# Kernel optimization log

Hardware: AMD Instinct MI355X
Metric: run time of the kernel (lower is better)

Reference implementation:

```python
import jax, jax.numpy as jnp
import numpy as np

N_HEAD = 8
N_INPUTS = 2
N_EMBD = 256
B, T1, T2 = 4, 8192, 8192


def setup_inputs() -> dict:
    key = jax.random.key(0)
    ks = jax.random.split(key, 8)
    s = 1.0 / np.sqrt(N_EMBD)
    return {
        "x": jax.random.normal(ks[0], (B, T1, N_EMBD), dtype=jnp.float32),
        "y": jax.random.normal(ks[1], (N_INPUTS, B, T2, N_EMBD), dtype=jnp.float32),
        "Wq": jax.random.normal(ks[2], (N_EMBD, N_EMBD), dtype=jnp.float32) * s,
        "bq": jnp.zeros((N_EMBD,), dtype=jnp.float32),
        "Wk": jax.random.normal(ks[3], (N_INPUTS, N_EMBD, N_EMBD), dtype=jnp.float32) * s,
        "bk": jnp.zeros((N_INPUTS, N_EMBD), dtype=jnp.float32),
        "Wv": jax.random.normal(ks[4], (N_INPUTS, N_EMBD, N_EMBD), dtype=jnp.float32) * s,
        "bv": jnp.zeros((N_INPUTS, N_EMBD), dtype=jnp.float32),
        "Wp": jax.random.normal(ks[5], (N_EMBD, N_EMBD), dtype=jnp.float32) * s,
        "bp": jnp.zeros((N_EMBD,), dtype=jnp.float32),
    }


def _split_heads(t):
    # [B, T, C] -> [B, H, T, d]
    Bt, Tt, C = t.shape
    return t.reshape(Bt, Tt, N_HEAD, C // N_HEAD).transpose(0, 2, 1, 3)


def reference(x, y, Wq, bq, Wk, bk, Wv, bv, Wp, bp):
    Bx, T, C = x.shape
    q = jax.nn.softmax(_split_heads(x @ Wq + bq), axis=-1)  # [B,H,T1,d]
    out = q  # faithful to original: out initialized to q
    for i in range(N_INPUTS):
        k = jax.nn.softmax(_split_heads(y[i] @ Wk[i] + bk[i]), axis=-1)  # [B,H,T2,d]
        v = _split_heads(y[i] @ Wv[i] + bv[i])                            # [B,H,T2,d]
        k_cumsum = k.sum(axis=-2, keepdims=True)                          # [B,H,1,d]
        D_inv = 1.0 / (q * k_cumsum).sum(axis=-1, keepdims=True)          # [B,H,T1,1]
        kv = jnp.einsum('bhtd,bhte->bhde', k, v)                          # [B,H,d,d]
        out = out + jnp.einsum('bhnd,bhde->bhne', q, kv) * D_inv
    # b h n d -> b n (h d)
    out = out.transpose(0, 2, 1, 3).reshape(Bx, T, C)
    return out @ Wp + bp
```

## Files before the change

### kernel.cpp

```cpp
#include <hip/hip_runtime.h>
#include <math.h>

#define NHEAD 8
#define CEMB  256
#define NIN   2
#define BB    4
#define TT    8192

typedef __attribute__((ext_vector_type(8))) short short8;
typedef __attribute__((ext_vector_type(4))) float f32x4;
typedef __attribute__((ext_vector_type(16))) float f32x16;

__device__ __forceinline__ unsigned short f2bf(float f) {
    union { float f; unsigned u; } v; v.f = f;
    unsigned u = v.u;
    return (unsigned short)((u + 0x7fffu + ((u >> 16) & 1u)) >> 16);
}
__device__ __forceinline__ float bf2f(unsigned short s) {
    union { unsigned u; float f; } v; v.u = ((unsigned)s) << 16;
    return v.f;
}

__global__ __launch_bounds__(256) void prep_w(const float* __restrict__ Wq,
    const float* __restrict__ Wk, const float* __restrict__ Wv,
    const float* __restrict__ Wp, unsigned short* __restrict__ wsb)
{
    int gid = blockIdx.x * 256 + threadIdx.x;
    int m = gid >> 16;
    int idx = gid & 65535;
    int n = idx >> 8, k = idx & 255;
    const float* src; unsigned short* dst;
    switch (m) {
        case 0: src = Wq;          dst = wsb;          break;
        case 1: src = Wk;          dst = wsb + 65536;  break;
        case 2: src = Wk + 65536;  dst = wsb + 131072; break;
        case 3: src = Wv;          dst = wsb + 196608; break;
        case 4: src = Wv + 65536;  dst = wsb + 262144; break;
        default: src = Wp;         dst = wsb + 327680; break;
    }
    dst[n * 256 + k] = f2bf(src[k * 256 + n]);
}

template<int ITERS>
__global__ __launch_bounds__(512, 2) void passA(const float* __restrict__ y,
    const float* __restrict__ bk, const float* __restrict__ bv,
    const unsigned short* __restrict__ Wkt, const unsigned short* __restrict__ Wvt,
    float* __restrict__ part)
{
    __shared__ unsigned short ytile[64][256];
    __shared__ unsigned short tr[8][32][68];

    const int i = blockIdx.z, b = blockIdx.y, x0 = blockIdx.x;
    const int tid = threadIdx.x;
    const int wid = tid >> 6, lane = tid & 63;
    const int lg = lane >> 4, li = lane & 15;
    const int l31 = lane & 31, hk = lane >> 5;
    const int h = wid, lm = li & 7;

    const float bk0 = bk[i * CEMB + h * 32 + li];
    const float bk1 = bk[i * CEMB + h * 32 + 16 + li];
    const float bv0 = bv[i * CEMB + h * 32 + li];
    const float bv1 = bv[i * CEMB + h * 32 + 16 + li];

    const unsigned short* wk0 = Wkt + ((size_t)(i * 256 + h * 32 + li)) * 256 + lg * 8;
    const unsigned short* wk1 = wk0 + 16 * 256;
    const unsigned short* wv0 = Wvt + ((size_t)(i * 256 + h * 32 + li)) * 256 + lg * 8;
    const unsigned short* wv1 = wv0 + 16 * 256;

    f32x16 kvacc = {};
    float ksa0 = 0.f, ksa1 = 0.f;

    #pragma unroll
    for (int iter = 0; iter < ITERS; ++iter) {
        __syncthreads();
        const int row0 = (x0 * ITERS + iter) * 64;
        const float* yb = y + ((size_t)(i * BB + b) * TT + row0) * CEMB;
        #pragma unroll
        for (int j = 0; j < 8; ++j) {
            int idx = tid + j * 512;
            int r = idx >> 6, c4 = (idx & 63) << 2;
            int sw = ((((c4 >> 3) ^ (r & 7)) << 3) | (c4 & 7));
            float4 v4 = *(const float4*)&yb[(size_t)r * CEMB + c4];
            ushort4 p; p.x = f2bf(v4.x); p.y = f2bf(v4.y); p.z = f2bf(v4.z); p.w = f2bf(v4.w);
            *(ushort4*)&ytile[r][sw] = p;
        }
        __syncthreads();

        f32x4 acc[4][2];
        #pragma unroll
        for (int rt = 0; rt < 4; ++rt) { acc[rt][0] = (f32x4){}; acc[rt][1] = (f32x4){}; }
        #pragma unroll 2
        for (int ks = 0; ks < 8; ++ks) {
            const int sw8 = (((4 * ks + lg) ^ lm) << 3);
            short8 a0 = *(const short8*)&ytile[li][sw8];
            short8 a1 = *(const short8*)&ytile[16 + li][sw8];
            short8 a2 = *(const short8*)&ytile[32 + li][sw8];
            short8 a3 = *(const short8*)&ytile[48 + li][sw8];
            short8 f0 = *(const short8*)(wk0 + ks * 32);
            short8 f1 = *(const short8*)(wk1 + ks * 32);
            acc[0][0] = __builtin_amdgcn_mfma_f32_16x16x32_bf16(a0, f0, acc[0][0], 0, 0, 0);
            acc[0][1] = __builtin_amdgcn_mfma_f32_16x16x32_bf16(a0, f1, acc[0][1], 0, 0, 0);
            acc[1][0] = __builtin_amdgcn_mfma_f32_16x16x32_bf16(a1, f0, acc[1][0], 0, 0, 0);
            acc[1][1] = __builtin_amdgcn_mfma_f32_16x16x32_bf16(a1, f1, acc[1][1], 0, 0, 0);
            acc[2][0] = __builtin_amdgcn_mfma_f32_16x16x32_bf16(a2, f0, acc[2][0], 0, 0, 0);
            acc[2][1] = __builtin_amdgcn_mfma_f32_16x16x32_bf16(a2, f1, acc[2][1], 0, 0, 0);
            acc[3][0] = __builtin_amdgcn_mfma_f32_16x16x32_bf16(a3, f0, acc[3][0], 0, 0, 0);
            acc[3][1] = __builtin_amdgcn_mfma_f32_16x16x32_bf16(a3, f1, acc[3][1], 0, 0, 0);
        }
        #pragma unroll
        for (int rt = 0; rt < 4; ++rt) {
            float kq0[4], kq1[4];
            #pragma unroll
            for (int reg = 0; reg < 4; ++reg) {
                float e0 = __expf(acc[rt][0][reg] + bk0);
                float e1 = __expf(acc[rt][1][reg] + bk1);
                float s = e0 + e1;
                s += __shfl_xor(s, 1, 16);
                s += __shfl_xor(s, 2, 16);
                s += __shfl_xor(s, 4, 16);
                s += __shfl_xor(s, 8, 16);
                float isv = 1.f / s;
                kq0[reg] = e0 * isv; kq1[reg] = e1 * isv;
                ksa0 += kq0[reg]; ksa1 += kq1[reg];
            }
            ushort4 p;
            p.x = f2bf(kq0[0]); p.y = f2bf(kq0[1]); p.z = f2bf(kq0[2]); p.w = f2bf(kq0[3]);
            *(ushort4*)&tr[wid][li][16 * rt + 4 * lg] = p;
            p.x = f2bf(kq1[0]); p.y = f2bf(kq1[1]); p.z = f2bf(kq1[2]); p.w = f2bf(kq1[3]);
            *(ushort4*)&tr[wid][16 + li][16 * rt + 4 * lg] = p;
        }
        #pragma unroll
        for (int rt = 0; rt < 4; ++rt) { acc[rt][0] = (f32x4){}; acc[rt][1] = (f32x4){}; }
        #pragma unroll 2
        for (int ks = 0; ks < 8; ++ks) {
            const int sw8 = (((4 * ks + lg) ^ lm) << 3);
            short8 a0 = *(const short8*)&ytile[li][sw8];
            short8 a1 = *(const short8*)&ytile[16 + li][sw8];
            short8 a2 = *(const short8*)&ytile[32 + li][sw8];
            short8 a3 = *(const short8*)&ytile[48 + li][sw8];
            short8 f0 = *(const short8*)(wv0 + ks * 32);
            short8 f1 = *(const short8*)(wv1 + ks * 32);
            acc[0][0] = __builtin_amdgcn_mfma_f32_16x16x32_bf16(a0, f0, acc[0][0], 0, 0, 0);
            acc[0][1] = __builtin_amdgcn_mfma_f32_16x16x32_bf16(a0, f1, acc[0][1], 0, 0, 0);
            acc[1][0] = __builtin_amdgcn_mfma_f32_16x16x32_bf16(a1, f0, acc[1][0], 0, 0, 0);
            acc[1][1] = __builtin_amdgcn_mfma_f32_16x16x32_bf16(a1, f1, acc[1][1], 0, 0, 0);
            acc[2][0] = __builtin_amdgcn_mfma_f32_16x16x32_bf16(a2, f0, acc[2][0], 0, 0, 0);
            acc[2][1] = __builtin_amdgcn_mfma_f32_16x16x32_bf16(a2, f1, acc[2][1], 0, 0, 0);
            acc[3][0] = __builtin_amdgcn_mfma_f32_16x16x32_bf16(a3, f0, acc[3][0], 0, 0, 0);
            acc[3][1] = __builtin_amdgcn_mfma_f32_16x16x32_bf16(a3, f1, acc[3][1], 0, 0, 0);
        }
        asm volatile("s_waitcnt lgkmcnt(0)" ::: "memory");
        short8 ka[4];
        #pragma unroll
        for (int ts = 0; ts < 4; ++ts)
            ka[ts] = *(const short8*)&tr[wid][l31][ts * 16 + hk * 8];
        asm volatile("s_waitcnt lgkmcnt(0)" ::: "memory");
        #pragma unroll
        for (int rt = 0; rt < 4; ++rt) {
            ushort4 p;
            p.x = f2bf(acc[rt][0][0] + bv0); p.y = f2bf(acc[rt][0][1] + bv0);
            p.z = f2bf(acc[rt][0][2] + bv0); p.w = f2bf(acc[rt][0][3] + bv0);
            *(ushort4*)&tr[wid][li][16 * rt + 4 * lg] = p;
            p.x = f2bf(acc[rt][1][0] + bv1); p.y = f2bf(acc[rt][1][1] + bv1);
            p.z = f2bf(acc[rt][1][2] + bv1); p.w = f2bf(acc[rt][1][3] + bv1);
            *(ushort4*)&tr[wid][16 + li][16 * rt + 4 * lg] = p;
        }
        asm volatile("s_waitcnt lgkmcnt(0)" ::: "memory");
        #pragma unroll
        for (int ts = 0; ts < 4; ++ts) {
            short8 vb = *(const short8*)&tr[wid][l31][ts * 16 + hk * 8];
            kvacc = __builtin_amdgcn_mfma_f32_32x32x16_bf16(ka[ts], vb, kvacc, 0, 0, 0);
        }
        asm volatile("s_waitcnt lgkmcnt(0)" ::: "memory");
    }

    const int slots = TT / (ITERS * 64);
    const size_t slot = (size_t)(i * BB + b) * slots + x0;
    float* pb = part + slot * (NHEAD * 1056) + (size_t)h * 1056;
    #pragma unroll
    for (int reg = 0; reg < 16; ++reg) {
        int d = (reg & 3) + 8 * (reg >> 2) + 4 * hk;
        pb[d * 32 + l31] = kvacc[reg];
    }
    float s0 = ksa0, s1 = ksa1;
    s0 += __shfl_xor(s0, 16, 64); s0 += __shfl_xor(s0, 32, 64);
    s1 += __shfl_xor(s1, 16, 64); s1 += __shfl_xor(s1, 32, 64);
    if (lg == 0) { pb[1024 + li] = s0; pb[1024 + 16 + li] = s1; }
}

__global__ __launch_bounds__(256) void reduceKV1(const float* __restrict__ part,
    float* __restrict__ part2, int slots)
{
    const int sc = blockIdx.x, g = blockIdx.y;
    const int ib = g >> 3, h = g & 7;
    const int tid = threadIdx.x;
    const float* p = part + ((size_t)(ib * slots + sc * 8) * NHEAD + h) * 1056;
    float* o = part2 + ((size_t)(sc * 64 + g)) * 1056;
    const size_t sstride = (size_t)NHEAD * 1056;
    for (int e = tid; e < 1056; e += 256) {
        float s = 0.f;
        #pragma unroll
        for (int xx = 0; xx < 8; ++xx) s += p[(size_t)xx * sstride + e];
        o[e] = s;
    }
}

__global__ __launch_bounds__(256) void reduceKV2(const float* __restrict__ part2,
    unsigned short* __restrict__ kvt, float* __restrict__ ksum, int nsc)
{
    const int g = blockIdx.x;
    const int tid = threadIdx.x;
    const size_t gstride = (size_t)64 * 1056;
    const float* p = part2 + (size_t)g * 1056;
    for (int e = tid; e < 1056; e += 256) {
        float s = 0.f;
        for (int sc = 0; sc < nsc; ++sc) s += p[(size_t)sc * gstride + e];
        if (e < 1024) kvt[(size_t)g * 1024 + (e & 31) * 32 + (e >> 5)] = f2bf(s);
        else          ksum[(size_t)g * 32 + (e - 1024)] = s;
    }
}

__global__ __launch_bounds__(512, 4) void passB(const float* __restrict__ x,
    const float* __restrict__ bq, const float* __restrict__ bp,
    const unsigned short* __restrict__ Wqt, const unsigned short* __restrict__ Wpt,
    const unsigned short* __restrict__ kvt, const float* __restrict__ ksum,
    float* __restrict__ out)
{
    __shared__ unsigned short xa[64][256];
    __shared__ unsigned short ql[64][256];
    __shared__ float dl[2][64][8];

    const int b = blockIdx.y, x0 = blockIdx.x;
    const int row0 = x0 * 64;
    const int tid = threadIdx.x;
    const int wid = tid >> 6, lane = tid & 63, lg = lane >> 4, li = lane & 15;
    const int h = wid, lm = li & 7;

    const float* xb = x + ((size_t)b * TT + row0) * CEMB;
    #pragma unroll
    for (int j = 0; j < 8; ++j) {
        int idx = tid + j * 512;
        int r = idx >> 6, c4 = (idx & 63) << 2;
        int sw = ((((c4 >> 3) ^ (r & 7)) << 3) | (c4 & 7));
        float4 v4 = *(const float4*)&xb[(size_t)r * CEMB + c4];
        ushort4 p; p.x = f2bf(v4.x); p.y = f2bf(v4.y); p.z = f2bf(v4.z); p.w = f2bf(v4.w);
        *(ushort4*)&xa[r][sw] = p;
    }
    __syncthreads();

    {
        f32x4 qa[4][2];
        #pragma unroll
        for (int rt = 0; rt < 4; ++rt) { qa[rt][0] = (f32x4){}; qa[rt][1] = (f32x4){}; }

        const unsigned short* wq0 = Wqt + ((size_t)(h * 32 + li)) * 256 + lg * 8;
        const unsigned short* wq1 = wq0 + 16 * 256;
        #pragma unroll 2
        for (int ks = 0; ks < 8; ++ks) {
            const int sw8 = (((4 * ks + lg) ^ lm) << 3);
            short8 a0 = *(const short8*)&xa[li][sw8];
            short8 a1 = *(const short8*)&xa[16 + li][sw8];
            short8 a2 = *(const short8*)&xa[32 + li][sw8];
            short8 a3 = *(const short8*)&xa[48 + li][sw8];
            short8 f0 = *(const short8*)(wq0 + ks * 32);
            short8 f1 = *(const short8*)(wq1 + ks * 32);
            qa[0][0] = __builtin_amdgcn_mfma_f32_16x16x32_bf16(a0, f0, qa[0][0], 0, 0, 0);
            qa[0][1] = __builtin_amdgcn_mfma_f32_16x16x32_bf16(a0, f1, qa[0][1], 0, 0, 0);
            qa[1][0] = __builtin_amdgcn_mfma_f32_16x16x32_bf16(a1, f0, qa[1][0], 0, 0, 0);
            qa[1][1] = __builtin_amdgcn_mfma_f32_16x16x32_bf16(a1, f1, qa[1][1], 0, 0, 0);
            qa[2][0] = __builtin_amdgcn_mfma_f32_16x16x32_bf16(a2, f0, qa[2][0], 0, 0, 0);
            qa[2][1] = __builtin_amdgcn_mfma_f32_16x16x32_bf16(a2, f1, qa[2][1], 0, 0, 0);
            qa[3][0] = __builtin_amdgcn_mfma_f32_16x16x32_bf16(a3, f0, qa[3][0], 0, 0, 0);
            qa[3][1] = __builtin_amdgcn_mfma_f32_16x16x32_bf16(a3, f1, qa[3][1], 0, 0, 0);
        }
        const float bq0 = bq[h * 32 + li];
        const float bq1 = bq[h * 32 + 16 + li];
        #pragma unroll
        for (int rt = 0; rt < 4; ++rt) {
            #pragma unroll
            for (int reg = 0; reg < 4; ++reg) {
                float e0 = __expf(qa[rt][0][reg] + bq0);
                float e1 = __expf(qa[rt][1][reg] + bq1);
                float s = e0 + e1;
                s += __shfl_xor(s, 1, 16);
                s += __shfl_xor(s, 2, 16);
                s += __shfl_xor(s, 4, 16);
                s += __shfl_xor(s, 8, 16);
                float isv = 1.f / s;
                int r = 16 * rt + 4 * lg + reg;
                int r7 = r & 7;
                int sw0 = (((4 * h + (li >> 3)) ^ r7) << 3) | lm;
                int sw1 = (((4 * h + 2 + (li >> 3)) ^ r7) << 3) | lm;
                ql[r][sw0] = f2bf(e0 * isv);
                ql[r][sw1] = f2bf(e1 * isv);
            }
        }
    }
    __syncthreads();

    {
        int r = tid >> 3, hh = tid & 7;
        const float* ks0 = ksum + ((size_t)(0 * BB + b) * 8 + hh) * 32;
        const float* ks1 = ksum + ((size_t)(1 * BB + b) * 8 + hh) * 32;
        float s0 = 0.f, s1 = 0.f;
        #pragma unroll
        for (int d8 = 0; d8 < 4; ++d8) {
            int cu = (((4 * hh + d8) ^ (r & 7)) << 3);
            #pragma unroll
            for (int dd = 0; dd < 8; ++dd) {
                float qv = bf2f(ql[r][cu + dd]);
                s0 += qv * ks0[d8 * 8 + dd];
                s1 += qv * ks1[d8 * 8 + dd];
            }
        }
        dl[0][r][hh] = 1.f / s0;
        dl[1][r][hh] = 1.f / s1;
    }
    __syncthreads();

    #pragma unroll
    for (int rt = 0; rt < 4; ++rt) {
        float of0[4], of1[4];
        #pragma unroll
        for (int reg = 0; reg < 4; ++reg) {
            int rk = (4 * lg + reg) & 7;
            int r = 16 * rt + 4 * lg + reg;
            int col0 = (((4 * h + (li >> 3)) ^ rk) << 3) | lm;
            int col1 = (((4 * h + 2 + (li >> 3)) ^ rk) << 3) | lm;
            of0[reg] = bf2f(ql[r][col0]);
            of1[reg] = bf2f(ql[r][col1]);
        }
        short8 af = *(const short8*)&ql[16 * rt + li][(((4 * h + lg) ^ lm) << 3)];
        #pragma unroll
        for (int ii = 0; ii < NIN; ++ii) {
            const unsigned short* kvb = kvt + ((size_t)((ii * BB + b) * 8 + h)) * 1024;
            short8 b0 = *(const short8*)(kvb + (size_t)li * 32 + lg * 8);
            short8 b1 = *(const short8*)(kvb + (size_t)(16 + li) * 32 + lg * 8);
            f32x4 z = {};
            f32x4 t0 = __builtin_amdgcn_mfma_f32_16x16x32_bf16(af, b0, z, 0, 0, 0);
            f32x4 t1 = __builtin_amdgcn_mfma_f32_16x16x32_bf16(af, b1, z, 0, 0, 0);
            #pragma unroll
            for (int reg = 0; reg < 4; ++reg) {
                float dv = dl[ii][16 * rt + 4 * lg + reg][h];
                of0[reg] += t0[reg] * dv;
                of1[reg] += t1[reg] * dv;
            }
        }
        #pragma unroll
        for (int reg = 0; reg < 4; ++reg) {
            int rk = (4 * lg + reg) & 7;
            int r = 16 * rt + 4 * lg + reg;
            int col0 = (((4 * h + (li >> 3)) ^ rk) << 3) | lm;
            int col1 = (((4 * h + 2 + (li >> 3)) ^ rk) << 3) | lm;
            xa[r][col0] = f2bf(of0[reg]);
            xa[r][col1] = f2bf(of1[reg]);
        }
    }
    __syncthreads();

    {
        f32x4 of[4][2];
        #pragma unroll
        for (int rt = 0; rt < 4; ++rt) { of[rt][0] = (f32x4){}; of[rt][1] = (f32x4){}; }
        const unsigned short* wp0 = Wpt + ((size_t)(h * 32 + li)) * 256 + lg * 8;
        const unsigned short* wp1 = wp0 + 16 * 256;
        #pragma unroll 2
        for (int ks = 0; ks < 8; ++ks) {
            const int sw8 = (((4 * ks + lg) ^ lm) << 3);
            short8 a0 = *(const short8*)&xa[li][sw8];
            short8 a1 = *(const short8*)&xa[16 + li][sw8];
            short8 a2 = *(const short8*)&xa[32 + li][sw8];
            short8 a3 = *(const short8*)&xa[48 + li][sw8];
            short8 f0 = *(const short8*)(wp0 + ks * 32);
            short8 f1 = *(const short8*)(wp1 + ks * 32);
            of[0][0] = __builtin_amdgcn_mfma_f32_16x16x32_bf16(a0, f0, of[0][0], 0, 0, 0);
            of[0][1] = __builtin_amdgcn_mfma_f32_16x16x32_bf16(a0, f1, of[0][1], 0, 0, 0);
            of[1][0] = __builtin_amdgcn_mfma_f32_16x16x32_bf16(a1, f0, of[1][0], 0, 0, 0);
            of[1][1] = __builtin_amdgcn_mfma_f32_16x16x32_bf16(a1, f1, of[1][1], 0, 0, 0);
            of[2][0] = __builtin_amdgcn_mfma_f32_16x16x32_bf16(a2, f0, of[2][0], 0, 0, 0);
            of[2][1] = __builtin_amdgcn_mfma_f32_16x16x32_bf16(a2, f1, of[2][1], 0, 0, 0);
            of[3][0] = __builtin_amdgcn_mfma_f32_16x16x32_bf16(a3, f0, of[3][0], 0, 0, 0);
            of[3][1] = __builtin_amdgcn_mfma_f32_16x16x32_bf16(a3, f1, of[3][1], 0, 0, 0);
        }
        const float bp0 = bp[h * 32 + li];
        const float bp1 = bp[h * 32 + 16 + li];
        #pragma unroll
        for (int rt = 0; rt < 4; ++rt) {
            #pragma unroll
            for (int reg = 0; reg < 4; ++reg) {
                int r = 16 * rt + 4 * lg + reg;
                float* ob = out + ((size_t)b * TT + row0 + r) * CEMB + h * 32;
                ob[li]      = of[rt][0][reg] + bp0;
                ob[16 + li] = of[rt][1][reg] + bp1;
            }
        }
    }
}

extern "C" void kernel_launch(void* const* d_in, const int* in_sizes, int n_in,
                              void* d_out, int out_size, void* d_ws, size_t ws_size,
                              hipStream_t stream)
{
    const float* x  = (const float*)d_in[0];
    const float* y  = (const float*)d_in[1];
    const float* Wq = (const float*)d_in[2];
    const float* bq = (const float*)d_in[3];
    const float* Wk = (const float*)d_in[4];
    const float* bk = (const float*)d_in[5];
    const float* Wv = (const float*)d_in[6];
    const float* bv = (const float*)d_in[7];
    const float* Wp = (const float*)d_in[8];
    const float* bp = (const float*)d_in[9];
    float* out = (float*)d_out;

    const size_t wbytes = 786432;
    int slots = 128;
    size_t partBytes  = (size_t)NIN * BB * slots * NHEAD * 1056 * 4;
    size_t part2Bytes = (size_t)(slots / 8) * 64 * 1056 * 4;
    if (wbytes + partBytes + part2Bytes + 131072 + 8192 > ws_size) {
        slots = 64;
        partBytes  = (size_t)NIN * BB * slots * NHEAD * 1056 * 4;
        part2Bytes = (size_t)(slots / 8) * 64 * 1056 * 4;
    }
    unsigned short* wsb = (unsigned short*)d_ws;
    float* part  = (float*)((char*)d_ws + wbytes);
    float* part2 = (float*)((char*)d_ws + wbytes + partBytes);
    unsigned short* kvt = (unsigned short*)((char*)d_ws + wbytes + partBytes + part2Bytes);
    float* ksum = (float*)((char*)d_ws + wbytes + partBytes + part2Bytes + 131072);

    hipLaunchKernelGGL(prep_w, dim3(1536), dim3(256), 0, stream, Wq, Wk, Wv, Wp, wsb);
    if (slots == 128)
        hipLaunchKernelGGL((passA<1>), dim3(128, BB, NIN), dim3(512), 0, stream,
                           y, bk, bv, wsb + 65536, wsb + 196608, part);
    else
        hipLaunchKernelGGL((passA<2>), dim3(64, BB, NIN), dim3(512), 0, stream,
                           y, bk, bv, wsb + 65536, wsb + 196608, part);
    hipLaunchKernelGGL(reduceKV1, dim3(slots / 8, 64), dim3(256), 0, stream, part, part2, slots);
    hipLaunchKernelGGL(reduceKV2, dim3(64), dim3(256), 0, stream, part2, kvt, ksum, slots / 8);
    hipLaunchKernelGGL(passB, dim3(128, BB), dim3(512), 0, stream,
                       x, bq, bp, wsb + 0, wsb + 327680, kvt, ksum, out);
}
```

Baseline: 119.5 us.

## Use passA<2> with 64 slots and merge two-stage KV reduction into one kernel

Always launches passA with ITERS=2 (64 row-chunks per batch) instead of picking 128 slots when the workspace allows, which halves the partial KV buffer. The two reduction kernels are replaced by one kernel that sums the 64 partials per (input, batch, head) directly, split into four element chunks per group. This removes a kernel launch and the intermediate part2 round trip, at the cost of fewer, longer passA blocks and a longer serial loop in each reduction thread.

```diff
diff --git a/kernel.cpp b/kernel.cpp
--- a/kernel.cpp
+++ b/kernel.cpp
@@ -188,33 +188,19 @@
     if (lg == 0) { pb[1024 + li] = s0; pb[1024 + 16 + li] = s1; }
 }
 
-__global__ __launch_bounds__(256) void reduceKV1(const float* __restrict__ part,
-    float* __restrict__ part2, int slots)
+__global__ __launch_bounds__(256) void reduceKV(const float* __restrict__ part,
+    unsigned short* __restrict__ kvt, float* __restrict__ ksum)
 {
-    const int sc = blockIdx.x, g = blockIdx.y;
+    const int g = blockIdx.y, ech = blockIdx.x;
     const int ib = g >> 3, h = g & 7;
     const int tid = threadIdx.x;
-    const float* p = part + ((size_t)(ib * slots + sc * 8) * NHEAD + h) * 1056;
-    float* o = part2 + ((size_t)(sc * 64 + g)) * 1056;
-    const size_t sstride = (size_t)NHEAD * 1056;
-    for (int e = tid; e < 1056; e += 256) {
+    const int e0 = ech * 264;
+    const int e1 = (e0 + 264 < 1056) ? e0 + 264 : 1056;
+    for (int e = e0 + tid; e < e1; e += 256) {
         float s = 0.f;
-        #pragma unroll
-        for (int xx = 0; xx < 8; ++xx) s += p[(size_t)xx * sstride + e];
-        o[e] = s;
-    }
-}
-
-__global__ __launch_bounds__(256) void reduceKV2(const float* __restrict__ part2,
-    unsigned short* __restrict__ kvt, float* __restrict__ ksum, int nsc)
-{
-    const int g = blockIdx.x;
-    const int tid = threadIdx.x;
-    const size_t gstride = (size_t)64 * 1056;
-    const float* p = part2 + (size_t)g * 1056;
-    for (int e = tid; e < 1056; e += 256) {
-        float s = 0.f;
-        for (int sc = 0; sc < nsc; ++sc) s += p[(size_t)sc * gstride + e];
+        const float* p = part + ((size_t)ib * 64 * NHEAD + h) * 1056 + e;
+        #pragma unroll 4
+        for (int xx = 0; xx < 64; ++xx) s += p[(size_t)xx * NHEAD * 1056];
         if (e < 1024) kvt[(size_t)g * 1024 + (e & 31) * 32 + (e >> 5)] = f2bf(s);
         else          ksum[(size_t)g * 32 + (e - 1024)] = s;
     }
@@ -413,30 +399,15 @@
     const float* bp = (const float*)d_in[9];
     float* out = (float*)d_out;
 
-    const size_t wbytes = 786432;
-    int slots = 128;
-    size_t partBytes  = (size_t)NIN * BB * slots * NHEAD * 1056 * 4;
-    size_t part2Bytes = (size_t)(slots / 8) * 64 * 1056 * 4;
-    if (wbytes + partBytes + part2Bytes + 131072 + 8192 > ws_size) {
-        slots = 64;
-        partBytes  = (size_t)NIN * BB * slots * NHEAD * 1056 * 4;
-        part2Bytes = (size_t)(slots / 8) * 64 * 1056 * 4;
-    }
     unsigned short* wsb = (unsigned short*)d_ws;
-    float* part  = (float*)((char*)d_ws + wbytes);
-    float* part2 = (float*)((char*)d_ws + wbytes + partBytes);
-    unsigned short* kvt = (unsigned short*)((char*)d_ws + wbytes + partBytes + part2Bytes);
-    float* ksum = (float*)((char*)d_ws + wbytes + partBytes + part2Bytes + 131072);
+    float* part = (float*)((char*)d_ws + 786432);
+    unsigned short* kvt = (unsigned short*)((char*)d_ws + 18087936);
+    float* ksum = (float*)((char*)d_ws + 18219008);
 
     hipLaunchKernelGGL(prep_w, dim3(1536), dim3(256), 0, stream, Wq, Wk, Wv, Wp, wsb);
-    if (slots == 128)
-        hipLaunchKernelGGL((passA<1>), dim3(128, BB, NIN), dim3(512), 0, stream,
-                           y, bk, bv, wsb + 65536, wsb + 196608, part);
-    else
-        hipLaunchKernelGGL((passA<2>), dim3(64, BB, NIN), dim3(512), 0, stream,
-                           y, bk, bv, wsb + 65536, wsb + 196608, part);
-    hipLaunchKernelGGL(reduceKV1, dim3(slots / 8, 64), dim3(256), 0, stream, part, part2, slots);
-    hipLaunchKernelGGL(reduceKV2, dim3(64), dim3(256), 0, stream, part2, kvt, ksum, slots / 8);
+    hipLaunchKernelGGL((passA<2>), dim3(64, BB, NIN), dim3(512), 0, stream,
+                       y, bk, bv, wsb + 65536, wsb + 196608, part);
+    hipLaunchKernelGGL(reduceKV, dim3(4, 64), dim3(256), 0, stream, part, kvt, ksum);
     hipLaunchKernelGGL(passB, dim3(128, BB), dim3(512), 0, stream,
                        x, bq, bp, wsb + 0, wsb + 327680, kvt, ksum, out);
 }
```

Result: faster. 110.4 us (-7.6%).
